# Kernel tuning notes

Hardware: AMD Instinct MI355X
Metric: run time of the kernel (lower is better)

Reference implementation:

```python
import jax, jax.numpy as jnp
import numpy as np

NB_HEAD = 8
HEAD_DIM = 64  # dim // nb_head = 512 // 8


def setup_inputs() -> dict:
    key = jax.random.key(0)
    ks = jax.random.split(key, 8)
    B, S, D = 4, 2048, 512
    scale = 1.0 / np.sqrt(D)
    return {
        "q_in": jax.random.normal(ks[0], (B, S, D), jnp.float32),
        "k_in": jax.random.normal(ks[1], (B, S, D), jnp.float32),
        "v_in": jax.random.normal(ks[2], (B, S, D), jnp.float32),
        "Wq": jax.random.normal(ks[3], (D, D), jnp.float32) * scale,
        "bq": jnp.zeros((D,), jnp.float32),
        "Wk": jax.random.normal(ks[4], (D, D), jnp.float32) * scale,
        "bk": jnp.zeros((D,), jnp.float32),
        "Wv": jax.random.normal(ks[5], (D, D), jnp.float32) * scale,
        "bv": jnp.zeros((D,), jnp.float32),
        "Wo": jax.random.normal(ks[6], (D, D), jnp.float32) * scale,
        "bo": jnp.zeros((D,), jnp.float32),
    }


def reference(q_in, k_in, v_in, Wq, bq, Wk, bk, Wv, bv, Wo, bo):
    B, Sq, D = q_in.shape
    Sk = k_in.shape[1]
    H, hd = NB_HEAD, HEAD_DIM

    # QKV projections, then split heads: [B, S, D] -> [B, H, S, hd]
    Q = (q_in @ Wq + bq).reshape(B, Sq, H, hd).transpose(0, 2, 1, 3)
    K = (k_in @ Wk + bk).reshape(B, Sk, H, hd).transpose(0, 2, 1, 3)
    V = (v_in @ Wv + bv).reshape(B, Sk, H, hd).transpose(0, 2, 1, 3)

    # scaled dot-product attention with causal mask (masked=True)
    scores = jnp.einsum("bhqd,bhkd->bhqk", Q, K) / jnp.sqrt(jnp.float32(hd))
    causal = jnp.tril(jnp.ones((Sq, Sk), dtype=bool))
    scores = jnp.where(causal, scores, -jnp.inf)
    probs = jax.nn.softmax(scores, axis=-1)
    attn = jnp.einsum("bhqk,bhkd->bhqd", probs, V)

    # merge heads and output projection
    out = attn.transpose(0, 2, 1, 3).reshape(B, Sq, D)
    return out @ Wo + bo
```

## Files before the change

### kernel.cpp

```cpp
#include <hip/hip_runtime.h>

typedef __attribute__((ext_vector_type(8))) short short8;
typedef __attribute__((ext_vector_type(4))) float f32x4;
typedef __attribute__((ext_vector_type(4))) unsigned short us4;

#define B_ 4
#define S_ 2048
#define D_ 512
#define H_ 8
#define HD_ 64

__device__ __forceinline__ unsigned short f2bf(float f) {
    unsigned int u = __float_as_uint(f);
    u += 0x7fffu + ((u >> 16) & 1u);
    return (unsigned short)(u >> 16);
}
__device__ __forceinline__ float bf2f(unsigned short h) {
    return __uint_as_float(((unsigned int)h) << 16);
}
__device__ __forceinline__ short8 ld8(const unsigned short* p) {
    return *reinterpret_cast<const short8*>(p);
}
__device__ __forceinline__ void async16(const unsigned short* g, unsigned short* l) {
    __builtin_amdgcn_global_load_lds(
        (const __attribute__((address_space(1))) void*)(const void*)g,
        (__attribute__((address_space(3))) void*)(void*)l, 16, 0, 0);
}

__global__ void detect_dtype(const unsigned short* __restrict__ q, int* __restrict__ flag) {
    __shared__ int cnt[256];
    int t = threadIdx.x;
    float x = bf2f(q[t]);
    float a = fabsf(x);
    cnt[t] = (a > 1e-5f && a < 1e3f) ? 1 : 0;
    __syncthreads();
    if (t == 0) {
        int s = 0;
        for (int i = 0; i < 256; i++) s += cnt[i];
        *flag = (s < 205) ? 1 : 0;
    }
}

__global__ __launch_bounds__(256) void cvt_bf16(
    const void* __restrict__ q, const void* __restrict__ k, const void* __restrict__ v,
    unsigned short* __restrict__ out, const int* __restrict__ flagp)
{
    int fl = *flagp;
    int z = blockIdx.z;
    const void* X = (z == 0) ? q : (z == 1) ? k : v;
    unsigned short* o = out + (size_t)z * 4194304;
    size_t i = ((size_t)blockIdx.x * 256 + threadIdx.x) * 4;
    if (fl) {
        f32x4 u = *(const f32x4*)((const float*)X + i);
        us4 r;
        r.x = f2bf(u[0]); r.y = f2bf(u[1]); r.z = f2bf(u[2]); r.w = f2bf(u[3]);
        *(us4*)(o + i) = r;
    } else {
        *(us4*)(o + i) = *(const us4*)((const unsigned short*)X + i);
    }
}

__global__ __launch_bounds__(256) void transpose512(
    const void* __restrict__ W0, const void* __restrict__ W1,
    const void* __restrict__ W2, const void* __restrict__ W3,
    unsigned short* __restrict__ outbase, const int* __restrict__ flagp)
{
    __shared__ unsigned short t[64][66];
    int fl = *flagp;
    const void* W = (blockIdx.z == 0) ? W0 : (blockIdx.z == 1) ? W1
                    : (blockIdx.z == 2) ? W2 : W3;
    unsigned short* o = outbase + (size_t)blockIdx.z * 262144;
    int k0 = blockIdx.x * 64, n0 = blockIdx.y * 64;
    int tx = threadIdx.x, ty = threadIdx.y;
#pragma unroll
    for (int r = 0; r < 16; r++) {
        int row = ty * 16 + r;
        size_t idx = (size_t)(k0 + row) * D_ + n0 + tx;
        float v = fl ? ((const float*)W)[idx] : bf2f(((const unsigned short*)W)[idx]);
        t[row][tx] = f2bf(v);
    }
    __syncthreads();
#pragma unroll
    for (int r = 0; r < 16; r++) {
        int row = ty * 16 + r;
        o[(size_t)(n0 + row) * D_ + k0 + tx] = t[tx][row];
    }
}

#define GEMM_BODY(Xp, WTp)                                                              \
    int tid = threadIdx.x;                                                              \
    int w = tid >> 6, lane = tid & 63, lm = lane & 15, quad = lane >> 4;                \
    int wm = (w & 1) * 64, wn = (w >> 1) * 64;                                          \
    int srow = w * 32 + (lane >> 2);                                                    \
    int clog = (lane & 3) ^ ((lane >> 3) & 3);        \
    int csw = quad ^ ((lm >> 1) & 3);                \
    const unsigned short* gA = (Xp) + (size_t)(m0 + srow) * D_ + clog * 8;              \
    const unsigned short* gB = (WTp) + (size_t)(n0 + srow) * D_ + clog * 8;             \
    unsigned short* lA = &Atile[(w * 32) * 32];                                         \
    unsigned short* lB = &Btile[(w * 32) * 32];                                         \
    f32x4 acc[4][4];                                                                    \
    _Pragma("unroll") for (int mt = 0; mt < 4; mt++)                                    \
        _Pragma("unroll") for (int nt = 0; nt < 4; nt++)                                \
            acc[mt][nt] = (f32x4){0.f, 0.f, 0.f, 0.f};                                  \
    for (int k0 = 0; k0 < D_; k0 += 32) {                                               \
        async16(gA + k0, lA);                                                           \
        async16(gA + k0 + (size_t)16 * D_, lA + 16 * 32);                               \
        async16(gB + k0, lB);                                                           \
        async16(gB + k0 + (size_t)16 * D_, lB + 16 * 32);                               \
        asm volatile("s_waitcnt vmcnt(0)" ::: "memory");                                \
        __syncthreads();                                                                \
        short8 af[4], bfr[4];                                                           \
        _Pragma("unroll") for (int mt = 0; mt < 4; mt++)                                \
            af[mt] = ld8(&Atile[(wm + mt * 16 + lm) * 32 + csw * 8]);                   \
        _Pragma("unroll") for (int nt = 0; nt < 4; nt++)                                \
            bfr[nt] = ld8(&Btile[(wn + nt * 16 + lm) * 32 + csw * 8]);                  \
        _Pragma("unroll") for (int mt = 0; mt < 4; mt++)                                \
            _Pragma("unroll") for (int nt = 0; nt < 4; nt++)                            \
                acc[mt][nt] = __builtin_amdgcn_mfma_f32_16x16x32_bf16(                  \
                    af[mt], bfr[nt], acc[mt][nt], 0, 0, 0);                             \
        __syncthreads();                                                                \
    }

__global__ __launch_bounds__(256) void gemm_qkv(
    const unsigned short* __restrict__ Xbf, const unsigned short* __restrict__ WTbase,
    const void* __restrict__ bq, const void* __restrict__ bk, const void* __restrict__ bv,
    unsigned short* __restrict__ Qw, unsigned short* __restrict__ Kw,
    unsigned short* __restrict__ Vw, const int* __restrict__ flagp)
{
    __shared__ __align__(16) unsigned short Atile[128 * 32];
    __shared__ __align__(16) unsigned short Btile[128 * 32];
    int z = blockIdx.z;
    const unsigned short* X = Xbf + (size_t)z * 4194304;
    const void* bias = (z == 0) ? bq : (z == 1) ? bk : bv;
    int fl = *flagp;
    int m0 = blockIdx.x * 128, n0 = blockIdx.y * 128;

    GEMM_BODY(X, WTbase + (size_t)z * 262144)

#pragma unroll
    for (int nt = 0; nt < 4; nt++) {
        int n = n0 + wn + nt * 16 + lm;
        float bv_ = fl ? ((const float*)bias)[n] : bf2f(((const unsigned short*)bias)[n]);
        int hh = n >> 6, d = n & 63;
#pragma unroll
        for (int mt = 0; mt < 4; mt++) {
#pragma unroll
            for (int r = 0; r < 4; r++) {
                int m = m0 + wm + mt * 16 + quad * 4 + r;
                int b = m >> 11, s = m & 2047;
                unsigned short hv = f2bf(acc[mt][nt][r] + bv_);
                if (z == 2)
                    Vw[((size_t)(b * H_ + hh) * HD_ + d) * S_ + s] = hv;
                else if (z == 1)
                    Kw[((size_t)(b * H_ + hh) * S_ + s) * HD_ + d] = hv;
                else
                    Qw[((size_t)(b * H_ + hh) * S_ + s) * HD_ + d] = hv;
            }
        }
    }
}

__global__ __launch_bounds__(256) void gemm_out(
    const unsigned short* __restrict__ Xa, const unsigned short* __restrict__ WT,
    const void* __restrict__ bias, float* __restrict__ out, const int* __restrict__ flagp)
{
    __shared__ __align__(16) unsigned short Atile[128 * 32];
    __shared__ __align__(16) unsigned short Btile[128 * 32];
    int fl = *flagp;
    int m0 = blockIdx.x * 128, n0 = blockIdx.y * 128;

    GEMM_BODY(Xa, WT)

#pragma unroll
    for (int nt = 0; nt < 4; nt++) {
        int n = n0 + wn + nt * 16 + lm;
        float bv_ = fl ? ((const float*)bias)[n] : bf2f(((const unsigned short*)bias)[n]);
#pragma unroll
        for (int mt = 0; mt < 4; mt++)
#pragma unroll
            for (int r = 0; r < 4; r++) {
                int m = m0 + wm + mt * 16 + quad * 4 + r;
                out[(size_t)m * D_ + n] = acc[mt][nt][r] + bv_;
            }
    }
}

__global__ __launch_bounds__(256) void attn_kernel(
    const unsigned short* __restrict__ Q, const unsigned short* __restrict__ K,
    const unsigned short* __restrict__ VT, unsigned short* __restrict__ ATT)
{
    __shared__ __align__(16) unsigned short Ktile[2][64 * 64];
    __shared__ __align__(16) unsigned short Vtile[2][64 * 64];
    __shared__ __align__(16) unsigned short Plds[4][2][16][68];
    int p = blockIdx.x, bh = blockIdx.y;
    int tid = threadIdx.x;
    int w = tid >> 6, lane = tid & 63, lm = lane & 15, quad = lane >> 4;

    const unsigned short* Qb = Q + (size_t)bh * S_ * HD_;
    const unsigned short* Kb = K + (size_t)bh * S_ * HD_;
    const unsigned short* Vb = VT + (size_t)bh * S_ * HD_;
    int b = bh >> 3, hh = bh & 7;

    int srow = lane >> 3;
    int lc = (lane & 7) ^ srow;
    int physA = quad ^ (lm & 7);
    int physB = (4 + quad) ^ (lm & 7);

#pragma unroll 1
    for (int half = 0; half < 2; half++) {
        int qt = half ? p : (31 - p);
        int q0 = qt * 64 + w * 16;

        __syncthreads();

        short8 aq0 = ld8(Qb + (size_t)(q0 + lm) * HD_ + quad * 8);
        short8 aq1 = ld8(Qb + (size_t)(q0 + lm) * HD_ + 32 + quad * 8);

#pragma unroll
        for (int i = 0; i < 2; i++) {
            int row = w * 16 + i * 8 + srow;
            async16(Kb + (size_t)row * HD_ + lc * 8, &Ktile[0][(w * 16 + i * 8) * 64]);
            async16(Vb + (size_t)row * S_ + lc * 8, &Vtile[0][(w * 16 + i * 8) * 64]);
        }

        f32x4 o[4];
#pragma unroll
        for (int nt = 0; nt < 4; nt++) o[nt] = (f32x4){0.f, 0.f, 0.f, 0.f};
        float mrow[4], lrow[4];
#pragma unroll
        for (int r = 0; r < 4; r++) { mrow[r] = -INFINITY; lrow[r] = 0.f; }

        for (int kt = 0; kt <= qt; kt++) {
            int cb = kt & 1;
            asm volatile("s_waitcnt vmcnt(0)" ::: "memory");
            __syncthreads();

            short8 kb0[4], kb1[4], vb0[4], vb1[4];
#pragma unroll
            for (int nt = 0; nt < 4; nt++) {
                kb0[nt] = ld8(&Ktile[cb][(nt * 16 + lm) * 64 + physA * 8]);
                kb1[nt] = ld8(&Ktile[cb][(nt * 16 + lm) * 64 + physB * 8]);
                vb0[nt] = ld8(&Vtile[cb][(nt * 16 + lm) * 64 + physA * 8]);
                vb1[nt] = ld8(&Vtile[cb][(nt * 16 + lm) * 64 + physB * 8]);
            }
            if (kt < qt) {
                int nb = cb ^ 1;
#pragma unroll
                for (int i = 0; i < 2; i++) {
                    int row = w * 16 + i * 8 + srow;
                    async16(Kb + (size_t)((kt + 1) * 64 + row) * HD_ + lc * 8,
                            &Ktile[nb][(w * 16 + i * 8) * 64]);
                    async16(Vb + (size_t)row * S_ + (kt + 1) * 64 + lc * 8,
                            &Vtile[nb][(w * 16 + i * 8) * 64]);
                }
            }

            f32x4 sc[4];
#pragma unroll
            for (int nt = 0; nt < 4; nt++) {
                f32x4 z = (f32x4){0.f, 0.f, 0.f, 0.f};
                z = __builtin_amdgcn_mfma_f32_16x16x32_bf16(aq0, kb0[nt], z, 0, 0, 0);
                z = __builtin_amdgcn_mfma_f32_16x16x32_bf16(aq1, kb1[nt], z, 0, 0, 0);
                sc[nt] = z;
            }
            bool diag = (kt == qt);
#pragma unroll
            for (int nt = 0; nt < 4; nt++) {
#pragma unroll
                for (int r = 0; r < 4; r++) {
                    float v = sc[nt][r] * 0.125f;
                    if (diag && (nt * 16 + lm > w * 16 + quad * 4 + r)) v = -INFINITY;
                    sc[nt][r] = v;
                }
            }
            float alpha[4];
#pragma unroll
            for (int r = 0; r < 4; r++) {
                float vm = fmaxf(fmaxf(sc[0][r], sc[1][r]), fmaxf(sc[2][r], sc[3][r]));
                vm = fmaxf(vm, __shfl_xor(vm, 1));
                vm = fmaxf(vm, __shfl_xor(vm, 2));
                vm = fmaxf(vm, __shfl_xor(vm, 4));
                vm = fmaxf(vm, __shfl_xor(vm, 8));
                float mn = fmaxf(mrow[r], vm);
                alpha[r] = __expf(mrow[r] - mn);
                mrow[r] = mn;
            }
#pragma unroll
            for (int nt = 0; nt < 4; nt++)
#pragma unroll
                for (int r = 0; r < 4; r++)
                    sc[nt][r] = __expf(sc[nt][r] - mrow[r]);
#pragma unroll
            for (int r = 0; r < 4; r++) {
                float s = sc[0][r] + sc[1][r] + sc[2][r] + sc[3][r];
                s += __shfl_xor(s, 1);
                s += __shfl_xor(s, 2);
                s += __shfl_xor(s, 4);
                s += __shfl_xor(s, 8);
                lrow[r] = lrow[r] * alpha[r] + s;
#pragma unroll
                for (int nt = 0; nt < 4; nt++) o[nt][r] *= alpha[r];
            }
            unsigned short (*Pb)[68] = Plds[w][cb];
#pragma unroll
            for (int nt = 0; nt < 4; nt++)
#pragma unroll
                for (int r = 0; r < 4; r++)
                    Pb[quad * 4 + r][nt * 16 + lm] = f2bf(sc[nt][r]);
            asm volatile("s_waitcnt lgkmcnt(0)" ::: "memory");
            __builtin_amdgcn_wave_barrier();
            short8 pa0 = ld8(&Pb[lm][quad * 8]);
            short8 pa1 = ld8(&Pb[lm][32 + quad * 8]);
#pragma unroll
            for (int nt = 0; nt < 4; nt++) {
                o[nt] = __builtin_amdgcn_mfma_f32_16x16x32_bf16(pa0, vb0[nt], o[nt], 0, 0, 0);
                o[nt] = __builtin_amdgcn_mfma_f32_16x16x32_bf16(pa1, vb1[nt], o[nt], 0, 0, 0);
            }
        }

#pragma unroll
        for (int r = 0; r < 4; r++) {
            float inv = (lrow[r] > 0.f) ? (1.0f / lrow[r]) : 0.f;
            int s = q0 + quad * 4 + r;
#pragma unroll
            for (int nt = 0; nt < 4; nt++)
                ATT[((size_t)b * S_ + s) * D_ + hh * 64 + nt * 16 + lm] = f2bf(o[nt][r] * inv);
        }
    }
}

extern "C" void kernel_launch(void* const* d_in, const int* in_sizes, int n_in,
                              void* d_out, int out_size, void* d_ws, size_t ws_size,
                              hipStream_t stream)
{
    const void* q_in = d_in[0];
    const void* k_in = d_in[1];
    const void* v_in = d_in[2];
    const void* Wq = d_in[3];
    const void* bq = d_in[4];
    const void* Wk = d_in[5];
    const void* bk = d_in[6];
    const void* Wv = d_in[7];
    const void* bv = d_in[8];
    const void* Wo = d_in[9];
    const void* bo = d_in[10];
    unsigned short* ws = (unsigned short*)d_ws;

    int* flag = (int*)d_ws;
    unsigned short* WqT = ws + 32;
    unsigned short* WkT = WqT + 262144;
    unsigned short* WvT = WkT + 262144;
    unsigned short* WoT = WvT + 262144;
    unsigned short* Xbf = WoT + 262144;
    unsigned short* Qw = Xbf + 12582912;
    unsigned short* Kw = Qw + 4194304;
    unsigned short* Vw = Kw + 4194304;
    unsigned short* Aw = Vw + 4194304;

    detect_dtype<<<1, 256, 0, stream>>>((const unsigned short*)q_in, flag);
    transpose512<<<dim3(8, 8, 4), dim3(64, 4), 0, stream>>>(Wq, Wk, Wv, Wo, WqT, flag);
    cvt_bf16<<<dim3(4096, 1, 3), 256, 0, stream>>>(q_in, k_in, v_in, Xbf, flag);
    gemm_qkv<<<dim3(64, 4, 3), 256, 0, stream>>>(Xbf, WqT, bq, bk, bv, Qw, Kw, Vw, flag);
    attn_kernel<<<dim3(16, 32), 256, 0, stream>>>(Qw, Kw, Vw, Aw);
    gemm_out<<<dim3(64, 4), 256, 0, stream>>>(Aw, WoT, bo, (float*)d_out, flag);
}
```

Measured before the change: 238.2 us.

## Fold softmax scale into Q, use exp2, MFMA row sums, deepen GEMM K-tile

Multiplies Q by 0.125·log2(e) in the QKV projection epilogue, so attention can drop the per-score scale and use exp2f instead of __expf. The softmax row sum is now computed with an MFMA against a vector of bf16 ones in place of the shuffle reductions. The P staging buffer in LDS goes from double- to single-buffered per wave. The projection GEMMs now use a 64-wide K tile with a new XOR swizzle, which halves the number of loop iterations and barriers at the cost of twice the LDS. Row sums now come from bf16-rounded probabilities, which slightly changes the numerics.

```diff
diff --git a/kernel.cpp b/kernel.cpp
--- a/kernel.cpp
+++ b/kernel.cpp
@@ -9,6 +9,7 @@
 #define D_ 512
 #define H_ 8
 #define HD_ 64
+#define QSCALE 0.1803368801111204f
 
 __device__ __forceinline__ unsigned short f2bf(float f) {
     unsigned int u = __float_as_uint(f);
@@ -91,33 +92,39 @@
     int tid = threadIdx.x;                                                              \
     int w = tid >> 6, lane = tid & 63, lm = lane & 15, quad = lane >> 4;                \
     int wm = (w & 1) * 64, wn = (w >> 1) * 64;                                          \
-    int srow = w * 32 + (lane >> 2);                                                    \
-    int clog = (lane & 3) ^ ((lane >> 3) & 3);        \
-    int csw = quad ^ ((lm >> 1) & 3);                \
-    const unsigned short* gA = (Xp) + (size_t)(m0 + srow) * D_ + clog * 8;              \
-    const unsigned short* gB = (WTp) + (size_t)(n0 + srow) * D_ + clog * 8;             \
-    unsigned short* lA = &Atile[(w * 32) * 32];                                         \
-    unsigned short* lB = &Btile[(w * 32) * 32];                                         \
+    int sr8 = lane >> 3;                                         \
+    int clog = (lane & 7) ^ sr8;                   \
+    int pA = quad ^ (lm & 7);                                 \
+    int pB = (4 + quad) ^ (lm & 7);                           \
+    const unsigned short* gA = (Xp) + (size_t)(m0 + w * 32 + sr8) * D_ + clog * 8;      \
+    const unsigned short* gB = (WTp) + (size_t)(n0 + w * 32 + sr8) * D_ + clog * 8;     \
     f32x4 acc[4][4];                                                                    \
     _Pragma("unroll") for (int mt = 0; mt < 4; mt++)                                    \
         _Pragma("unroll") for (int nt = 0; nt < 4; nt++)                                \
             acc[mt][nt] = (f32x4){0.f, 0.f, 0.f, 0.f};                                  \
-    for (int k0 = 0; k0 < D_; k0 += 32) {                                               \
-        async16(gA + k0, lA);                                                           \
-        async16(gA + k0 + (size_t)16 * D_, lA + 16 * 32);                               \
-        async16(gB + k0, lB);                                                           \
-        async16(gB + k0 + (size_t)16 * D_, lB + 16 * 32);                               \
+    for (int k0 = 0; k0 < D_; k0 += 64) {                                               \
+        _Pragma("unroll") for (int i = 0; i < 4; i++) {                                 \
+            async16(gA + k0 + (size_t)(i * 8) * D_, &Atile[(w * 32 + i * 8) * 64]);     \
+            async16(gB + k0 + (size_t)(i * 8) * D_, &Btile[(w * 32 + i * 8) * 64]);     \
+        }                                                                               \
         asm volatile("s_waitcnt vmcnt(0)" ::: "memory");                                \
         __syncthreads();                                                                \
-        short8 af[4], bfr[4];                                                           \
+        short8 af[4][2], bfr[4][2];                                                     \
+        _Pragma("unroll") for (int mt = 0; mt < 4; mt++) {                              \
+            af[mt][0] = ld8(&Atile[(wm + mt * 16 + lm) * 64 + pA * 8]);                 \
+            af[mt][1] = ld8(&Atile[(wm + mt * 16 + lm) * 64 + pB * 8]);                 \
+        }                                                                               \
+        _Pragma("unroll") for (int nt = 0; nt < 4; nt++) {                              \
+            bfr[nt][0] = ld8(&Btile[(wn + nt * 16 + lm) * 64 + pA * 8]);                \
+            bfr[nt][1] = ld8(&Btile[(wn + nt * 16 + lm) * 64 + pB * 8]);                \
+        }                                                                               \
         _Pragma("unroll") for (int mt = 0; mt < 4; mt++)                                \
-            af[mt] = ld8(&Atile[(wm + mt * 16 + lm) * 32 + csw * 8]);                   \
-        _Pragma("unroll") for (int nt = 0; nt < 4; nt++)                                \
-            bfr[nt] = ld8(&Btile[(wn + nt * 16 + lm) * 32 + csw * 8]);                  \
-        _Pragma("unroll") for (int mt = 0; mt < 4; mt++)                                \
-            _Pragma("unroll") for (int nt = 0; nt < 4; nt++)                            \
+            _Pragma("unroll") for (int nt = 0; nt < 4; nt++) {                          \
                 acc[mt][nt] = __builtin_amdgcn_mfma_f32_16x16x32_bf16(                  \
-                    af[mt], bfr[nt], acc[mt][nt], 0, 0, 0);                             \
+                    af[mt][0], bfr[nt][0], acc[mt][nt], 0, 0, 0);                       \
+                acc[mt][nt] = __builtin_amdgcn_mfma_f32_16x16x32_bf16(                  \
+                    af[mt][1], bfr[nt][1], acc[mt][nt], 0, 0, 0);                       \
+            }                                                                           \
         __syncthreads();                                                                \
     }
 
@@ -127,8 +134,8 @@
     unsigned short* __restrict__ Qw, unsigned short* __restrict__ Kw,
     unsigned short* __restrict__ Vw, const int* __restrict__ flagp)
 {
-    __shared__ __align__(16) unsigned short Atile[128 * 32];
-    __shared__ __align__(16) unsigned short Btile[128 * 32];
+    __shared__ __align__(16) unsigned short Atile[128 * 64];
+    __shared__ __align__(16) unsigned short Btile[128 * 64];
     int z = blockIdx.z;
     const unsigned short* X = Xbf + (size_t)z * 4194304;
     const void* bias = (z == 0) ? bq : (z == 1) ? bk : bv;
@@ -137,6 +144,7 @@
 
     GEMM_BODY(X, WTbase + (size_t)z * 262144)
 
+    float osc = (z == 0) ? QSCALE : 1.0f;
 #pragma unroll
     for (int nt = 0; nt < 4; nt++) {
         int n = n0 + wn + nt * 16 + lm;
@@ -148,7 +156,7 @@
             for (int r = 0; r < 4; r++) {
                 int m = m0 + wm + mt * 16 + quad * 4 + r;
                 int b = m >> 11, s = m & 2047;
-                unsigned short hv = f2bf(acc[mt][nt][r] + bv_);
+                unsigned short hv = f2bf((acc[mt][nt][r] + bv_) * osc);
                 if (z == 2)
                     Vw[((size_t)(b * H_ + hh) * HD_ + d) * S_ + s] = hv;
                 else if (z == 1)
@@ -164,8 +172,8 @@
     const unsigned short* __restrict__ Xa, const unsigned short* __restrict__ WT,
     const void* __restrict__ bias, float* __restrict__ out, const int* __restrict__ flagp)
 {
-    __shared__ __align__(16) unsigned short Atile[128 * 32];
-    __shared__ __align__(16) unsigned short Btile[128 * 32];
+    __shared__ __align__(16) unsigned short Atile[128 * 64];
+    __shared__ __align__(16) unsigned short Btile[128 * 64];
     int fl = *flagp;
     int m0 = blockIdx.x * 128, n0 = blockIdx.y * 128;
 
@@ -191,7 +199,7 @@
 {
     __shared__ __align__(16) unsigned short Ktile[2][64 * 64];
     __shared__ __align__(16) unsigned short Vtile[2][64 * 64];
-    __shared__ __align__(16) unsigned short Plds[4][2][16][68];
+    __shared__ __align__(16) unsigned short Plds[4][16][68];
     int p = blockIdx.x, bh = blockIdx.y;
     int tid = threadIdx.x;
     int w = tid >> 6, lane = tid & 63, lm = lane & 15, quad = lane >> 4;
@@ -205,6 +213,10 @@
     int lc = (lane & 7) ^ srow;
     int physA = quad ^ (lm & 7);
     int physB = (4 + quad) ^ (lm & 7);
+
+    short8 vones;
+#pragma unroll
+    for (int j = 0; j < 8; j++) vones[j] = (short)0x3F80;
 
 #pragma unroll 1
     for (int half = 0; half < 2; half++) {
@@ -264,14 +276,12 @@
                 sc[nt] = z;
             }
             bool diag = (kt == qt);
-#pragma unroll
-            for (int nt = 0; nt < 4; nt++) {
-#pragma unroll
-                for (int r = 0; r < 4; r++) {
-                    float v = sc[nt][r] * 0.125f;
-                    if (diag && (nt * 16 + lm > w * 16 + quad * 4 + r)) v = -INFINITY;
-                    sc[nt][r] = v;
-                }
+            if (diag) {
+#pragma unroll
+                for (int nt = 0; nt < 4; nt++)
+#pragma unroll
+                    for (int r = 0; r < 4; r++)
+                        if (nt * 16 + lm > w * 16 + quad * 4 + r) sc[nt][r] = -INFINITY;
             }
             float alpha[4];
 #pragma unroll
@@ -282,26 +292,20 @@
                 vm = fmaxf(vm, __shfl_xor(vm, 4));
                 vm = fmaxf(vm, __shfl_xor(vm, 8));
                 float mn = fmaxf(mrow[r], vm);
-                alpha[r] = __expf(mrow[r] - mn);
+                alpha[r] = exp2f(mrow[r] - mn);
                 mrow[r] = mn;
             }
 #pragma unroll
             for (int nt = 0; nt < 4; nt++)
 #pragma unroll
                 for (int r = 0; r < 4; r++)
-                    sc[nt][r] = __expf(sc[nt][r] - mrow[r]);
-#pragma unroll
-            for (int r = 0; r < 4; r++) {
-                float s = sc[0][r] + sc[1][r] + sc[2][r] + sc[3][r];
-                s += __shfl_xor(s, 1);
-                s += __shfl_xor(s, 2);
-                s += __shfl_xor(s, 4);
-                s += __shfl_xor(s, 8);
-                lrow[r] = lrow[r] * alpha[r] + s;
+                    sc[nt][r] = exp2f(sc[nt][r] - mrow[r]);
+#pragma unroll
+            for (int r = 0; r < 4; r++)
 #pragma unroll
                 for (int nt = 0; nt < 4; nt++) o[nt][r] *= alpha[r];
-            }
-            unsigned short (*Pb)[68] = Plds[w][cb];
+
+            unsigned short (*Pb)[68] = Plds[w];
 #pragma unroll
             for (int nt = 0; nt < 4; nt++)
 #pragma unroll
@@ -311,11 +315,19 @@
             __builtin_amdgcn_wave_barrier();
             short8 pa0 = ld8(&Pb[lm][quad * 8]);
             short8 pa1 = ld8(&Pb[lm][32 + quad * 8]);
+
+            f32x4 lr = (f32x4){0.f, 0.f, 0.f, 0.f};
+            lr = __builtin_amdgcn_mfma_f32_16x16x32_bf16(pa0, vones, lr, 0, 0, 0);
+            lr = __builtin_amdgcn_mfma_f32_16x16x32_bf16(pa1, vones, lr, 0, 0, 0);
+
 #pragma unroll
             for (int nt = 0; nt < 4; nt++) {
                 o[nt] = __builtin_amdgcn_mfma_f32_16x16x32_bf16(pa0, vb0[nt], o[nt], 0, 0, 0);
                 o[nt] = __builtin_amdgcn_mfma_f32_16x16x32_bf16(pa1, vb1[nt], o[nt], 0, 0, 0);
             }
+#pragma unroll
+            for (int r = 0; r < 4; r++)
+                lrow[r] = lrow[r] * alpha[r] + lr[r];
         }
 
 #pragma unroll
```

Result: no change. 242.3 us (+1.7%).
